# Performance work log

Measured on AMD Instinct MI355X. Metric: run time of the kernel, lower is better.

Reference implementation:

```python
import jax, jax.numpy as jnp
import numpy as np

B, N, C, H = 4, 1024, 768, 12
D = C // H
SCALE = D ** -0.5


def setup_inputs() -> dict:
    key = jax.random.key(0)
    k1, k2, k3, k4 = jax.random.split(key, 4)
    x1 = jax.random.normal(k1, (B, N, C), dtype=jnp.float32)
    x2 = jax.random.normal(k2, (B, N, C), dtype=jnp.float32)
    # shared (dual-stream) Linear2 weights, torch nn.Linear layout: [out, in]
    W_qkv = jax.random.normal(k3, (3 * C, C), dtype=jnp.float32) * (C ** -0.5)
    b_qkv = jnp.zeros((3 * C,), dtype=jnp.float32)
    W_proj = jax.random.normal(k4, (C, C), dtype=jnp.float32) * (C ** -0.5)
    b_proj = jnp.zeros((C,), dtype=jnp.float32)
    return {"x1": x1, "x2": x2, "W_qkv": W_qkv, "b_qkv": b_qkv,
            "W_proj": W_proj, "b_proj": b_proj}


def _split_qkv(x, W_qkv, b_qkv):
    qkv = (x @ W_qkv.T + b_qkv).reshape(B, N, 3, H, D)
    qkv = jnp.transpose(qkv, (2, 0, 3, 1, 4))  # [3,B,H,N,D]
    return qkv[0], qkv[1], qkv[2]


def reference(x1, x2, W_qkv, b_qkv, W_proj, b_proj):
    q1, k1, v1 = _split_qkv(x1, W_qkv, b_qkv)
    q2, k2, v2 = _split_qkv(x2, W_qkv, b_qkv)
    # two score maps, combined before a single shared softmax
    s1 = jnp.einsum("bhqd,bhkd->bhqk", q1 * SCALE, k1)
    s2 = jnp.einsum("bhqd,bhkd->bhqk", q2 * SCALE, k2)
    attn = jax.nn.softmax(s1 + s2, axis=-1)  # [B,H,N,N]
    # same attention matrix applied to both value streams
    o1 = jnp.einsum("bhqk,bhkd->bhqd", attn, v1)
    o2 = jnpum = jnp.einsum("bhqk,bhkd->bhqd", attn, v2) if False else jnp.einsum("bhqk,bhkd->bhqd", attn, v2)
    o1 = jnp.transpose(o1, (0, 2, 1, 3)).reshape(B, N, C)
    o2 = jnp.transpose(o2, (0, 2, 1, 3)).reshape(B, N, C)
    y1 = o1 @ W_proj.T + b_proj
    y2 = o2 @ W_proj.T + b_proj
    return y1, y2
```

## Files before the change

kernel.cpp:

```cpp
#include <hip/hip_runtime.h>
#include <hip/hip_bf16.h>


typedef __bf16 bf16x8 __attribute__((ext_vector_type(8)));
typedef __bf16 bf16x4 __attribute__((ext_vector_type(4)));
typedef float  f32x4  __attribute__((ext_vector_type(4)));

__device__ __forceinline__ bf16x8 cvt8(const float* p) {
    f32x4 f0 = *(const f32x4*)p;
    f32x4 f1 = *(const f32x4*)(p + 4);
    bf16x8 r;
    r[0] = (__bf16)f0[0]; r[1] = (__bf16)f0[1]; r[2] = (__bf16)f0[2]; r[3] = (__bf16)f0[3];
    r[4] = (__bf16)f1[0]; r[5] = (__bf16)f1[1]; r[6] = (__bf16)f1[2]; r[7] = (__bf16)f1[3];
    return r;
}

__device__ __forceinline__ void async16(const __bf16* g, __bf16* l) {
    __builtin_amdgcn_global_load_lds(
        (const __attribute__((address_space(1))) void*)g,
        (__attribute__((address_space(3))) void*)l, 16, 0, 0);
}

__global__ __launch_bounds__(256)
void cvt3_k(const float* __restrict__ x1, const float* __restrict__ x2,
            const float* __restrict__ wq, __bf16* __restrict__ xc,
            __bf16* __restrict__ wqc)
{
    int bid = blockIdx.x;
    const float* src; __bf16* dst; int i;
    if (bid < 1536)      { src = x1; dst = xc;             i = (bid * 256 + threadIdx.x) * 8; }
    else if (bid < 3072) { src = x2; dst = xc + 3145728;   i = ((bid - 1536) * 256 + threadIdx.x) * 8; }
    else                 { src = wq; dst = wqc;            i = ((bid - 3072) * 256 + threadIdx.x) * 8; }
    *(bf16x8*)(dst + i) = cvt8(src + i);
}

__global__ __launch_bounds__(256)
void cvt_k(const float* __restrict__ src, __bf16* __restrict__ dst, int n) {
    int i = (blockIdx.x * 256 + threadIdx.x) * 8;
    if (i < n) *(bf16x8*)(dst + i) = cvt8(src + i);
}

__global__ __launch_bounds__(256)
void gemm_qkv_s(const __bf16* __restrict__ Xc, const __bf16* __restrict__ Wq,
                const float* __restrict__ bias,
                __bf16* __restrict__ qo, __bf16* __restrict__ ko,
                __bf16* __restrict__ vo)
{
    constexpr int K = 768;
    __shared__ __bf16 As[3][128 * 32];
    __shared__ __bf16 Bs[3][128 * 32];

    const int t = threadIdx.x, w = t >> 6, lane = t & 63;
    const int l15 = lane & 15, quad = lane >> 4;
    const int wm = w >> 1, wn = w & 1;

    const int bid  = blockIdx.x;
    const int xcd  = bid & 7;
    const int i6   = bid >> 3;
    const int pair = i6 / 18;
    const int gx   = i6 - pair * 18;
    const int p    = xcd * 8 + pair;
    const int gy   = p & 31;
    const int st   = p >> 5;

    const int lrow = lane >> 2, lcol = (lane & 3) * 8;

    const __bf16* Ab = Xc + (size_t)st * 3145728 + (size_t)(gy * 128) * K;
    const __bf16* Bb = Wq + (size_t)(gx * 128) * K;

    f32x4 acc[4][4];
#pragma unroll
    for (int mi = 0; mi < 4; mi++)
#pragma unroll
        for (int ni = 0; ni < 4; ni++) acc[mi][ni] = f32x4{0.f, 0.f, 0.f, 0.f};

#pragma unroll
    for (int i = 0; i < 2; i++) {
        int r = w * 32 + i * 16 + lrow;
        async16(Ab + (size_t)r * K + lcol, &As[0][r * 32 + lcol]);
        async16(Bb + (size_t)r * K + lcol, &Bs[0][r * 32 + lcol]);
    }

#pragma unroll 3
    for (int kt = 0; kt < 24; kt++) {
        const int cb = kt % 3;
        if (kt < 23) {
            const int nb = (kt + 1) % 3;
            const int k0 = (kt + 1) * 32;
#pragma unroll
            for (int i = 0; i < 2; i++) {
                int r = w * 32 + i * 16 + lrow;
                async16(Ab + (size_t)r * K + k0 + lcol, &As[nb][r * 32 + lcol]);
                async16(Bb + (size_t)r * K + k0 + lcol, &Bs[nb][r * 32 + lcol]);
            }
            asm volatile("s_waitcnt vmcnt(4)" ::: "memory");
        } else {
            asm volatile("s_waitcnt vmcnt(0)" ::: "memory");
        }
        __builtin_amdgcn_s_barrier();
        __builtin_amdgcn_sched_barrier(0);

        bf16x8 af[4], bfr[4];
#pragma unroll
        for (int mi = 0; mi < 4; mi++)
            af[mi] = *(const bf16x8*)&As[cb][(wm * 64 + mi * 16 + l15) * 32 + quad * 8];
#pragma unroll
        for (int ni = 0; ni < 4; ni++)
            bfr[ni] = *(const bf16x8*)&Bs[cb][(wn * 64 + ni * 16 + l15) * 32 + quad * 8];
#pragma unroll
        for (int mi = 0; mi < 4; mi++)
#pragma unroll
            for (int ni = 0; ni < 4; ni++)
                acc[mi][ni] = __builtin_amdgcn_mfma_f32_16x16x32_bf16(af[mi], bfr[ni], acc[mi][ni], 0, 0, 0);
    }

    const int which = (gx * 128) / 768;

    if (which == 2) {
#pragma unroll
        for (int ni = 0; ni < 4; ni++) {
            int j = gx * 128 + wn * 64 + ni * 16 + l15;
            int c = j - 1536;
            int h = c >> 6, d = c & 63;
            float bj = bias[j];
#pragma unroll
            for (int mi = 0; mi < 4; mi++) {
                int row0 = gy * 128 + wm * 64 + mi * 16 + quad * 4;
                int b = row0 >> 10, tok0 = row0 & 1023;
                bf16x4 pv;
#pragma unroll
                for (int r = 0; r < 4; r++) pv[r] = (__bf16)(acc[mi][ni][r] + bj);
                *(bf16x4*)&vo[((size_t)((st * 4 + b) * 12 + h) * 64 + d) * 1024 + tok0] = pv;
            }
        }
    } else {
#pragma unroll
        for (int ni = 0; ni < 4; ni++) {
            int j     = gx * 128 + wn * 64 + ni * 16 + l15;
            int c     = j - which * 768;
            int h = c >> 6, d = c & 63;
            float bj  = bias[j];
#pragma unroll
            for (int mi = 0; mi < 4; mi++) {
#pragma unroll
                for (int r = 0; r < 4; r++) {
                    int row = gy * 128 + wm * 64 + mi * 16 + quad * 4 + r;
                    int b = row >> 10, tok = row & 1023;
                    float val = acc[mi][ni][r] + bj;
                    if (which == 0)
                        qo[((size_t)((st * 4 + b) * 12 + h) * 1024 + tok) * 64 + d] = (__bf16)(val * 0.125f);
                    else
                        ko[((size_t)((st * 4 + b) * 12 + h) * 1024 + tok) * 64 + d] = (__bf16)val;
                }
            }
        }
    }
}

__global__ __launch_bounds__(256)
void gemm_proj(const __bf16* __restrict__ A, const __bf16* __restrict__ Wp,
               const float* __restrict__ bias, float* __restrict__ out)
{
    constexpr int K = 768;
    __shared__ __bf16 As[3][128 * 32];
    __shared__ __bf16 Bs[3][128 * 32];

    const int t = threadIdx.x, w = t >> 6, lane = t & 63;
    const int l15 = lane & 15, quad = lane >> 4;
    const int wm = w >> 1, wn = w & 1;
    const int gx = blockIdx.x, gy = blockIdx.y;
    const int lrow = lane >> 2, lcol = (lane & 3) * 8;

    const __bf16* Ab = A  + (size_t)(gy * 128) * K;
    const __bf16* Bb = Wp + (size_t)(gx * 128) * K;

    f32x4 acc[4][4];
#pragma unroll
    for (int mi = 0; mi < 4; mi++)
#pragma unroll
        for (int ni = 0; ni < 4; ni++) acc[mi][ni] = f32x4{0.f, 0.f, 0.f, 0.f};

#pragma unroll
    for (int i = 0; i < 2; i++) {
        int r = w * 32 + i * 16 + lrow;
        async16(Ab + (size_t)r * K + lcol, &As[0][r * 32 + lcol]);
        async16(Bb + (size_t)r * K + lcol, &Bs[0][r * 32 + lcol]);
    }

#pragma unroll 3
    for (int kt = 0; kt < 24; kt++) {
        const int cb = kt % 3;
        if (kt < 23) {
            const int nb = (kt + 1) % 3;
            const int k0 = (kt + 1) * 32;
#pragma unroll
            for (int i = 0; i < 2; i++) {
                int r = w * 32 + i * 16 + lrow;
                async16(Ab + (size_t)r * K + k0 + lcol, &As[nb][r * 32 + lcol]);
                async16(Bb + (size_t)r * K + k0 + lcol, &Bs[nb][r * 32 + lcol]);
            }
            asm volatile("s_waitcnt vmcnt(4)" ::: "memory");
        } else {
            asm volatile("s_waitcnt vmcnt(0)" ::: "memory");
        }
        __builtin_amdgcn_s_barrier();
        __builtin_amdgcn_sched_barrier(0);

        bf16x8 af[4], bfr[4];
#pragma unroll
        for (int mi = 0; mi < 4; mi++)
            af[mi] = *(const bf16x8*)&As[cb][(wm * 64 + mi * 16 + l15) * 32 + quad * 8];
#pragma unroll
        for (int ni = 0; ni < 4; ni++)
            bfr[ni] = *(const bf16x8*)&Bs[cb][(wn * 64 + ni * 16 + l15) * 32 + quad * 8];
#pragma unroll
        for (int mi = 0; mi < 4; mi++)
#pragma unroll
            for (int ni = 0; ni < 4; ni++)
                acc[mi][ni] = __builtin_amdgcn_mfma_f32_16x16x32_bf16(af[mi], bfr[ni], acc[mi][ni], 0, 0, 0);
    }

#pragma unroll
    for (int ni = 0; ni < 4; ni++) {
        int col  = gx * 128 + wn * 64 + ni * 16 + l15;
        float bj = bias[col];
#pragma unroll
        for (int mi = 0; mi < 4; mi++)
#pragma unroll
            for (int r = 0; r < 4; r++) {
                int row = gy * 128 + wm * 64 + mi * 16 + quad * 4 + r;
                out[(size_t)row * 768 + col] = acc[mi][ni][r] + bj;
            }
    }
}

__global__ __launch_bounds__(128, 2)
void attn_k(const __bf16* __restrict__ qws, const __bf16* __restrict__ kws,
            const __bf16* __restrict__ vws, __bf16* __restrict__ ows)
{
    __shared__ __bf16 Ks[2][2][2][2][512];
    __shared__ __bf16 Vs[2][2][4][512];
    __shared__ __bf16 Ps[2][2][16 * 72];

    const int g  = blockIdx.x;
    const int qt = g / 48;
    const int bh = g % 48;
    const int b = bh / 12, h = bh % 12;
    const int t = threadIdx.x, w = t >> 6, lane = t & 63;
    const int l15 = lane & 15, quad = lane >> 4;

    const size_t head_off = (size_t)bh * 65536;
    const size_t ss       = (size_t)48 * 65536;

    bf16x8 qf[2][2][2];
#pragma unroll
    for (int set = 0; set < 2; set++)
#pragma unroll
        for (int s = 0; s < 2; s++)
#pragma unroll
            for (int kk = 0; kk < 2; kk++)
                qf[set][s][kk] = *(const bf16x8*)(qws + s * ss + head_off
                    + (size_t)(qt * 64 + w * 32 + set * 16 + l15) * 64 + kk * 32 + quad * 8);

    float lsum[2] = {0.f, 0.f};
    f32x4 accO[2][2][4];
#pragma unroll
    for (int set = 0; set < 2; set++)
#pragma unroll
        for (int s = 0; s < 2; s++)
#pragma unroll
            for (int mi = 0; mi < 4; mi++) accO[set][s][mi] = f32x4{0.f, 0.f, 0.f, 0.f};

    const __bf16* kbase = kws + head_off;
    const __bf16* vbase = vws + head_off;

#define STAGE_TILE(BUF, KEYB)                                                   \
    do {                                                                        \
        if (w == 0) {                                                           \
            _Pragma("unroll")                                                   \
            for (int i = 0; i < 8; i++) {                                       \
                const int s = i >> 2, kk = (i >> 1) & 1, mi = i & 1;            \
                async16(kbase + s * ss + (size_t)((KEYB) + mi * 16 + l15) * 64  \
                            + kk * 32 + quad * 8,                               \
                        &Ks[BUF][s][kk][mi][lane * 8]);                         \
            }                                                                   \
        } else {                                                                \
            _Pragma("unroll")                                                   \
            for (int i = 0; i < 8; i++) {                                       \
                const int s = i >> 2, mi = i & 3;                               \
                async16(vbase + s * ss + (size_t)(mi * 16 + l15) * 1024         \
                            + (KEYB) + quad * 8,                                \
                        &Vs[BUF][s][mi][lane * 8]);                             \
            }                                                                   \
        }                                                                       \
    } while (0)

    STAGE_TILE(0, 0);
    __syncthreads();

#pragma unroll 2
    for (int kt = 0; kt < 32; kt++) {
        const int cb = kt & 1, nb = cb ^ 1;

        if (kt < 31) STAGE_TILE(nb, (kt + 1) * 32);

        f32x4 accS[2][2];
#pragma unroll
        for (int set = 0; set < 2; set++)
#pragma unroll
            for (int mi = 0; mi < 2; mi++) accS[set][mi] = f32x4{0.f, 0.f, 0.f, 0.f};
        __builtin_amdgcn_s_setprio(1);
#pragma unroll
        for (int s = 0; s < 2; s++)
#pragma unroll
            for (int kk = 0; kk < 2; kk++) {
                bf16x8 kf0 = *(const bf16x8*)&Ks[cb][s][kk][0][lane * 8];
                bf16x8 kf1 = *(const bf16x8*)&Ks[cb][s][kk][1][lane * 8];
#pragma unroll
                for (int set = 0; set < 2; set++) {
                    accS[set][0] = __builtin_amdgcn_mfma_f32_16x16x32_bf16(kf0, qf[set][s][kk], accS[set][0], 0, 0, 0);
                    accS[set][1] = __builtin_amdgcn_mfma_f32_16x16x32_bf16(kf1, qf[set][s][kk], accS[set][1], 0, 0, 0);
                }
            }
        __builtin_amdgcn_s_setprio(0);

#pragma unroll
        for (int set = 0; set < 2; set++) {
            float rs = 0.f;
#pragma unroll
            for (int mi = 0; mi < 2; mi++) {
                bf16x4 pk;
#pragma unroll
                for (int r = 0; r < 4; r++) {
                    float pv = __expf(accS[set][mi][r]);
                    pk[r] = (__bf16)pv;
                    rs += pv;
                }
                *(bf16x4*)&Ps[w][set][l15 * 72 + mi * 16 + quad * 4] = pk;
            }
            lsum[set] += rs;
        }

        bf16x8 pa0 = *(const bf16x8*)&Ps[w][0][l15 * 72 + quad * 8];
        bf16x8 pa1 = *(const bf16x8*)&Ps[w][1][l15 * 72 + quad * 8];
        __builtin_amdgcn_s_setprio(1);
#pragma unroll
        for (int s = 0; s < 2; s++)
#pragma unroll
            for (int mi = 0; mi < 4; mi++) {
                bf16x8 vf = *(const bf16x8*)&Vs[cb][s][mi][lane * 8];
                accO[0][s][mi] = __builtin_amdgcn_mfma_f32_16x16x32_bf16(vf, pa0, accO[0][s][mi], 0, 0, 0);
                accO[1][s][mi] = __builtin_amdgcn_mfma_f32_16x16x32_bf16(vf, pa1, accO[1][s][mi], 0, 0, 0);
            }
        __builtin_amdgcn_s_setprio(0);

        __syncthreads();
    }
#undef STAGE_TILE

#pragma unroll
    for (int set = 0; set < 2; set++) {
        float l = lsum[set];
        l += __shfl_xor(l, 16);
        l += __shfl_xor(l, 32);
        float il = 1.f / l;

        const int tok = qt * 64 + w * 32 + set * 16 + l15;
#pragma unroll
        for (int s = 0; s < 2; s++)
#pragma unroll
            for (int mi = 0; mi < 4; mi++) {
                bf16x4 ov;
#pragma unroll
                for (int r = 0; r < 4; r++) ov[r] = (__bf16)(accO[set][s][mi][r] * il);
                *(bf16x4*)&ows[((size_t)((s * 4 + b) * 1024 + tok)) * 768
                               + h * 64 + mi * 16 + quad * 4] = ov;
            }
    }
}

extern "C" void kernel_launch(void* const* d_in, const int* in_sizes, int n_in,
                              void* d_out, int out_size, void* d_ws, size_t ws_size,
                              hipStream_t stream)
{
    const float* x1    = (const float*)d_in[0];
    const float* x2    = (const float*)d_in[1];
    const float* Wqkv  = (const float*)d_in[2];
    const float* bqkv  = (const float*)d_in[3];
    const float* Wproj = (const float*)d_in[4];
    const float* bproj = (const float*)d_in[5];
    float* out = (float*)d_out;

    const size_t qkv_elems = (size_t)2 * 4 * 12 * 1024 * 64;
    __bf16* q_ws = (__bf16*)d_ws;
    __bf16* k_ws = q_ws + qkv_elems;
    __bf16* v_ws = k_ws + qkv_elems;
    __bf16* pool = v_ws + qkv_elems;
    __bf16* Wqc  = pool + 3145728;
    __bf16* o_ws = pool;
    __bf16* Wpc  = q_ws;
    __bf16* Xc   = (__bf16*)d_out;

    cvt3_k<<<3936, 256, 0, stream>>>(x1, x2, Wqkv, Xc, Wqc);
    gemm_qkv_s<<<1152, 256, 0, stream>>>(Xc, Wqc, bqkv, q_ws, k_ws, v_ws);
    attn_k<<<768, 128, 0, stream>>>(q_ws, k_ws, v_ws, o_ws);
    cvt_k<<<288, 256, 0, stream>>>(Wproj, Wpc, 589824);
    gemm_proj<<<dim3(6, 64), 256, 0, stream>>>(o_ws, Wpc, bproj, out);
}
```

Baseline: 214.0 us.

## Deepen GEMM pipelines to four stages and fold proj-weight conversion into first kernel

Both GEMM kernels move from a 3-buffer, prefetch-distance-1 pipeline to a 4-buffer pipeline that prefetches two k-tiles ahead, with the waitcnt thresholds adjusted to match. This should hide more global-load latency at the cost of more LDS per block, which may reduce occupancy. Separately, when the workspace is large enough, the W_proj fp32-to-bf16 conversion moves into the initial conversion kernel, removing one kernel launch before the projection GEMM.

Result: no change. 211.9 us (-1.0%).

```diff
diff --git a/kernel.cpp b/kernel.cpp
--- a/kernel.cpp
+++ b/kernel.cpp
@@ -22,15 +22,17 @@
 }
 
 __global__ __launch_bounds__(256)
-void cvt3_k(const float* __restrict__ x1, const float* __restrict__ x2,
-            const float* __restrict__ wq, __bf16* __restrict__ xc,
-            __bf16* __restrict__ wqc)
+void cvt4_k(const float* __restrict__ x1, const float* __restrict__ x2,
+            const float* __restrict__ wq, const float* __restrict__ wp,
+            __bf16* __restrict__ xc, __bf16* __restrict__ wqc,
+            __bf16* __restrict__ wpc)
 {
     int bid = blockIdx.x;
     const float* src; __bf16* dst; int i;
     if (bid < 1536)      { src = x1; dst = xc;             i = (bid * 256 + threadIdx.x) * 8; }
     else if (bid < 3072) { src = x2; dst = xc + 3145728;   i = ((bid - 1536) * 256 + threadIdx.x) * 8; }
-    else                 { src = wq; dst = wqc;            i = ((bid - 3072) * 256 + threadIdx.x) * 8; }
+    else if (bid < 3936) { src = wq; dst = wqc;            i = ((bid - 3072) * 256 + threadIdx.x) * 8; }
+    else                 { src = wp; dst = wpc;            i = ((bid - 3936) * 256 + threadIdx.x) * 8; }
     *(bf16x8*)(dst + i) = cvt8(src + i);
 }
 
@@ -47,8 +49,8 @@
                 __bf16* __restrict__ vo)
 {
     constexpr int K = 768;
-    __shared__ __bf16 As[3][128 * 32];
-    __shared__ __bf16 Bs[3][128 * 32];
+    __shared__ __bf16 As[4][128 * 32];
+    __shared__ __bf16 Bs[4][128 * 32];
 
     const int t = threadIdx.x, w = t >> 6, lane = t & 63;
     const int l15 = lane & 15, quad = lane >> 4;
@@ -74,25 +76,27 @@
 #pragma unroll
         for (int ni = 0; ni < 4; ni++) acc[mi][ni] = f32x4{0.f, 0.f, 0.f, 0.f};
 
-#pragma unroll
-    for (int i = 0; i < 2; i++) {
-        int r = w * 32 + i * 16 + lrow;
-        async16(Ab + (size_t)r * K + lcol, &As[0][r * 32 + lcol]);
-        async16(Bb + (size_t)r * K + lcol, &Bs[0][r * 32 + lcol]);
-    }
-
-#pragma unroll 3
+#define QSTAGE(BUF, KT)                                                         \
+    do {                                                                        \
+        const int _k0 = (KT) * 32;                                              \
+        _Pragma("unroll")                                                       \
+        for (int i = 0; i < 2; i++) {                                           \
+            int r = w * 32 + i * 16 + lrow;                                     \
+            async16(Ab + (size_t)r * K + _k0 + lcol, &As[BUF][r * 32 + lcol]);  \
+            async16(Bb + (size_t)r * K + _k0 + lcol, &Bs[BUF][r * 32 + lcol]);  \
+        }                                                                       \
+    } while (0)
+
+    QSTAGE(0, 0);
+    QSTAGE(1, 1);
+
+#pragma unroll 4
     for (int kt = 0; kt < 24; kt++) {
-        const int cb = kt % 3;
-        if (kt < 23) {
-            const int nb = (kt + 1) % 3;
-            const int k0 = (kt + 1) * 32;
-#pragma unroll
-            for (int i = 0; i < 2; i++) {
-                int r = w * 32 + i * 16 + lrow;
-                async16(Ab + (size_t)r * K + k0 + lcol, &As[nb][r * 32 + lcol]);
-                async16(Bb + (size_t)r * K + k0 + lcol, &Bs[nb][r * 32 + lcol]);
-            }
+        const int cb = kt & 3;
+        if (kt < 22) {
+            QSTAGE((kt + 2) & 3, kt + 2);
+            asm volatile("s_waitcnt vmcnt(8)" ::: "memory");
+        } else if (kt == 22) {
             asm volatile("s_waitcnt vmcnt(4)" ::: "memory");
         } else {
             asm volatile("s_waitcnt vmcnt(0)" ::: "memory");
@@ -113,6 +117,7 @@
             for (int ni = 0; ni < 4; ni++)
                 acc[mi][ni] = __builtin_amdgcn_mfma_f32_16x16x32_bf16(af[mi], bfr[ni], acc[mi][ni], 0, 0, 0);
     }
+#undef QSTAGE
 
     const int which = (gx * 128) / 768;
 
@@ -162,8 +167,8 @@
                const float* __restrict__ bias, float* __restrict__ out)
 {
     constexpr int K = 768;
-    __shared__ __bf16 As[3][128 * 32];
-    __shared__ __bf16 Bs[3][128 * 32];
+    __shared__ __bf16 As[4][128 * 32];
+    __shared__ __bf16 Bs[4][128 * 32];
 
     const int t = threadIdx.x, w = t >> 6, lane = t & 63;
     const int l15 = lane & 15, quad = lane >> 4;
@@ -180,25 +185,27 @@
 #pragma unroll
         for (int ni = 0; ni < 4; ni++) acc[mi][ni] = f32x4{0.f, 0.f, 0.f, 0.f};
 
-#pragma unroll
-    for (int i = 0; i < 2; i++) {
-        int r = w * 32 + i * 16 + lrow;
-        async16(Ab + (size_t)r * K + lcol, &As[0][r * 32 + lcol]);
-        async16(Bb + (size_t)r * K + lcol, &Bs[0][r * 32 + lcol]);
-    }
-
-#pragma unroll 3
+#define PSTAGE(BUF, KT)                                                         \
+    do {                                                                        \
+        const int _k0 = (KT) * 32;                                              \
+        _Pragma("unroll")                                                       \
+        for (int i = 0; i < 2; i++) {                                           \
+            int r = w * 32 + i * 16 + lrow;                                     \
+            async16(Ab + (size_t)r * K + _k0 + lcol, &As[BUF][r * 32 + lcol]);  \
+            async16(Bb + (size_t)r * K + _k0 + lcol, &Bs[BUF][r * 32 + lcol]);  \
+        }                                                                       \
+    } while (0)
+
+    PSTAGE(0, 0);
+    PSTAGE(1, 1);
+
+#pragma unroll 4
     for (int kt = 0; kt < 24; kt++) {
-        const int cb = kt % 3;
-        if (kt < 23) {
-            const int nb = (kt + 1) % 3;
-            const int k0 = (kt + 1) * 32;
-#pragma unroll
-            for (int i = 0; i < 2; i++) {
-                int r = w * 32 + i * 16 + lrow;
-                async16(Ab + (size_t)r * K + k0 + lcol, &As[nb][r * 32 + lcol]);
-                async16(Bb + (size_t)r * K + k0 + lcol, &Bs[nb][r * 32 + lcol]);
-            }
+        const int cb = kt & 3;
+        if (kt < 22) {
+            PSTAGE((kt + 2) & 3, kt + 2);
+            asm volatile("s_waitcnt vmcnt(8)" ::: "memory");
+        } else if (kt == 22) {
             asm volatile("s_waitcnt vmcnt(4)" ::: "memory");
         } else {
             asm volatile("s_waitcnt vmcnt(0)" ::: "memory");
@@ -219,6 +226,7 @@
             for (int ni = 0; ni < 4; ni++)
                 acc[mi][ni] = __builtin_amdgcn_mfma_f32_16x16x32_bf16(af[mi], bfr[ni], acc[mi][ni], 0, 0, 0);
     }
+#undef PSTAGE
 
 #pragma unroll
     for (int ni = 0; ni < 4; ni++) {
@@ -398,12 +406,15 @@
     __bf16* pool = v_ws + qkv_elems;
     __bf16* Wqc  = pool + 3145728;
     __bf16* o_ws = pool;
-    __bf16* Wpc  = q_ws;
     __bf16* Xc   = (__bf16*)d_out;
 
-    cvt3_k<<<3936, 256, 0, stream>>>(x1, x2, Wqkv, Xc, Wqc);
+    const bool big = ws_size >= (size_t)(4 * qkv_elems + 589824) * sizeof(__bf16);
+    __bf16* Wpc = big ? (pool + qkv_elems)
+                      : q_ws;
+
+    cvt4_k<<<big ? 4224 : 3936, 256, 0, stream>>>(x1, x2, Wqkv, Wproj, Xc, Wqc, Wpc);
     gemm_qkv_s<<<1152, 256, 0, stream>>>(Xc, Wqc, bqkv, q_ws, k_ws, v_ws);
     attn_k<<<768, 128, 0, stream>>>(q_ws, k_ws, v_ws, o_ws);
-    cvt_k<<<288, 256, 0, stream>>>(Wproj, Wpc, 589824);
+    if (!big) cvt_k<<<288, 256, 0, stream>>>(Wproj, Wpc, 589824);
     gemm_proj<<<dim3(6, 64), 256, 0, stream>>>(o_ws, Wpc, bproj, out);
 }
```

## Use 256x256 tiles with 8-wave pipelined QKV GEMM and fold proj weight cast

Applied to the files above, without the earlier changes.

The QKV projection GEMM moves from 128x128 tiles with 4 waves to 256x256 tiles with 8 waves. It uses a 4-deep LDS buffer with staggered A/B staging, split half-steps and s_setprio around the MFMA blocks, aiming for more operand reuse and better overlap of loads with compute. When the workspace is large enough, the W_proj bf16 conversion is folded into the first conversion kernel, which removes one launch. The grid shrinks to 288 blocks, which may leave CUs underfilled, and the larger LDS footprint limits occupancy.

New measurement: 222.9 us. +4.2%, slower.

```diff
diff --git a/kernel.cpp b/kernel.cpp
--- a/kernel.cpp
+++ b/kernel.cpp
@@ -22,15 +22,17 @@
 }
 
 __global__ __launch_bounds__(256)
-void cvt3_k(const float* __restrict__ x1, const float* __restrict__ x2,
-            const float* __restrict__ wq, __bf16* __restrict__ xc,
-            __bf16* __restrict__ wqc)
+void cvt4_k(const float* __restrict__ x1, const float* __restrict__ x2,
+            const float* __restrict__ wq, const float* __restrict__ wp,
+            __bf16* __restrict__ xc, __bf16* __restrict__ wqc,
+            __bf16* __restrict__ wpc)
 {
     int bid = blockIdx.x;
     const float* src; __bf16* dst; int i;
     if (bid < 1536)      { src = x1; dst = xc;             i = (bid * 256 + threadIdx.x) * 8; }
     else if (bid < 3072) { src = x2; dst = xc + 3145728;   i = ((bid - 1536) * 256 + threadIdx.x) * 8; }
-    else                 { src = wq; dst = wqc;            i = ((bid - 3072) * 256 + threadIdx.x) * 8; }
+    else if (bid < 3936) { src = wq; dst = wqc;            i = ((bid - 3072) * 256 + threadIdx.x) * 8; }
+    else                 { src = wp; dst = wpc;            i = ((bid - 3936) * 256 + threadIdx.x) * 8; }
     *(bf16x8*)(dst + i) = cvt8(src + i);
 }
 
@@ -40,92 +42,125 @@
     if (i < n) *(bf16x8*)(dst + i) = cvt8(src + i);
 }
 
-__global__ __launch_bounds__(256)
-void gemm_qkv_s(const __bf16* __restrict__ Xc, const __bf16* __restrict__ Wq,
-                const float* __restrict__ bias,
-                __bf16* __restrict__ qo, __bf16* __restrict__ ko,
-                __bf16* __restrict__ vo)
+__global__ __launch_bounds__(512, 2)
+void gemm_qkv_8p(const __bf16* __restrict__ Xc, const __bf16* __restrict__ Wq,
+                 const float* __restrict__ bias,
+                 __bf16* __restrict__ qo, __bf16* __restrict__ ko,
+                 __bf16* __restrict__ vo)
 {
     constexpr int K = 768;
-    __shared__ __bf16 As[3][128 * 32];
-    __shared__ __bf16 Bs[3][128 * 32];
+    __shared__ __bf16 As[4][256 * 32];
+    __shared__ __bf16 Bs[4][256 * 32];
 
     const int t = threadIdx.x, w = t >> 6, lane = t & 63;
     const int l15 = lane & 15, quad = lane >> 4;
-    const int wm = w >> 1, wn = w & 1;
-
-    const int bid  = blockIdx.x;
-    const int xcd  = bid & 7;
-    const int i6   = bid >> 3;
-    const int pair = i6 / 18;
-    const int gx   = i6 - pair * 18;
-    const int p    = xcd * 8 + pair;
-    const int gy   = p & 31;
-    const int st   = p >> 5;
-
-    const int lrow = lane >> 2, lcol = (lane & 3) * 8;
-
-    const __bf16* Ab = Xc + (size_t)st * 3145728 + (size_t)(gy * 128) * K;
-    const __bf16* Bb = Wq + (size_t)(gx * 128) * K;
-
-    f32x4 acc[4][4];
-#pragma unroll
-    for (int mi = 0; mi < 4; mi++)
+    const int wm = w >> 2, wn = w & 3;
+
+    const int bid = blockIdx.x;
+    const int xcd = bid & 7;
+    const int i6  = bid >> 3;
+    const int gy  = xcd * 4 + i6 / 9;
+    const int gx  = i6 % 9;
+    const int st  = gy >> 4;
+    const int gyl = gy & 15;
+
+    const int srow = t >> 2, scol = (t & 3) * 8;
+
+    const __bf16* Ab = Xc + (size_t)st * 3145728 + (size_t)(gyl * 256) * K;
+    const __bf16* Bb = Wq + (size_t)(gx * 256) * K;
+
+    f32x4 acc[8][4];
+#pragma unroll
+    for (int mi = 0; mi < 8; mi++)
 #pragma unroll
         for (int ni = 0; ni < 4; ni++) acc[mi][ni] = f32x4{0.f, 0.f, 0.f, 0.f};
 
-#pragma unroll
-    for (int i = 0; i < 2; i++) {
-        int r = w * 32 + i * 16 + lrow;
-        async16(Ab + (size_t)r * K + lcol, &As[0][r * 32 + lcol]);
-        async16(Bb + (size_t)r * K + lcol, &Bs[0][r * 32 + lcol]);
-    }
-
-#pragma unroll 3
-    for (int kt = 0; kt < 24; kt++) {
-        const int cb = kt % 3;
-        if (kt < 23) {
-            const int nb = (kt + 1) % 3;
-            const int k0 = (kt + 1) * 32;
-#pragma unroll
-            for (int i = 0; i < 2; i++) {
-                int r = w * 32 + i * 16 + lrow;
-                async16(Ab + (size_t)r * K + k0 + lcol, &As[nb][r * 32 + lcol]);
-                async16(Bb + (size_t)r * K + k0 + lcol, &Bs[nb][r * 32 + lcol]);
-            }
-            asm volatile("s_waitcnt vmcnt(4)" ::: "memory");
-        } else {
-            asm volatile("s_waitcnt vmcnt(0)" ::: "memory");
-        }
-        __builtin_amdgcn_s_barrier();
-        __builtin_amdgcn_sched_barrier(0);
-
-        bf16x8 af[4], bfr[4];
-#pragma unroll
-        for (int mi = 0; mi < 4; mi++)
-            af[mi] = *(const bf16x8*)&As[cb][(wm * 64 + mi * 16 + l15) * 32 + quad * 8];
-#pragma unroll
-        for (int ni = 0; ni < 4; ni++)
-            bfr[ni] = *(const bf16x8*)&Bs[cb][(wn * 64 + ni * 16 + l15) * 32 + quad * 8];
-#pragma unroll
-        for (int mi = 0; mi < 4; mi++)
+#define STG_A(BF, K0)                                                            \
+    do {                                                                         \
+        async16(Ab + (size_t)srow * K + (K0) + scol,                             \
+                &As[BF][srow * 32 + scol]);                                      \
+        async16(Ab + (size_t)(128 + srow) * K + (K0) + scol,                     \
+                &As[BF][(128 + srow) * 32 + scol]);                              \
+    } while (0)
+#define STG_B(BF, K0)                                                            \
+    do {                                                                         \
+        async16(Bb + (size_t)srow * K + (K0) + scol,                             \
+                &Bs[BF][srow * 32 + scol]);                                      \
+        async16(Bb + (size_t)(128 + srow) * K + (K0) + scol,                     \
+                &Bs[BF][(128 + srow) * 32 + scol]);                              \
+    } while (0)
+
+    STG_A(0, 0); STG_B(0, 0);
+    STG_A(1, 32); STG_B(1, 32);
+    asm volatile("s_waitcnt vmcnt(4)" ::: "memory");
+    __builtin_amdgcn_s_barrier();
+    __builtin_amdgcn_sched_barrier(0);
+
+#pragma unroll 4
+    for (int g = 0; g < 24; g++) {
+        const int bf = g & 3;
+        const int sb = (g + 2) & 3;
+        const int sk = (g + 2) * 32;
+        bf16x8 bfr[4];
+
+        {
+            bf16x8 af[4];
+#pragma unroll
+            for (int mi = 0; mi < 4; mi++)
+                af[mi] = *(const bf16x8*)&As[bf][(wm * 128 + mi * 16 + l15) * 32 + quad * 8];
 #pragma unroll
             for (int ni = 0; ni < 4; ni++)
-                acc[mi][ni] = __builtin_amdgcn_mfma_f32_16x16x32_bf16(af[mi], bfr[ni], acc[mi][ni], 0, 0, 0);
-    }
-
-    const int which = (gx * 128) / 768;
+                bfr[ni] = *(const bf16x8*)&Bs[bf][(wn * 64 + ni * 16 + l15) * 32 + quad * 8];
+            if (g < 22) STG_A(sb, sk);
+            __builtin_amdgcn_s_barrier();
+            __builtin_amdgcn_sched_barrier(0);
+            __builtin_amdgcn_s_setprio(1);
+#pragma unroll
+            for (int mi = 0; mi < 4; mi++)
+#pragma unroll
+                for (int ni = 0; ni < 4; ni++)
+                    acc[mi][ni] = __builtin_amdgcn_mfma_f32_16x16x32_bf16(af[mi], bfr[ni], acc[mi][ni], 0, 0, 0);
+            __builtin_amdgcn_s_setprio(0);
+            __builtin_amdgcn_s_barrier();
+            __builtin_amdgcn_sched_barrier(0);
+        }
+
+        {
+            bf16x8 af[4];
+#pragma unroll
+            for (int mi = 0; mi < 4; mi++)
+                af[mi] = *(const bf16x8*)&As[bf][(wm * 128 + 64 + mi * 16 + l15) * 32 + quad * 8];
+            if (g < 22) STG_B(sb, sk);
+            __builtin_amdgcn_s_barrier();
+            __builtin_amdgcn_sched_barrier(0);
+            __builtin_amdgcn_s_setprio(1);
+#pragma unroll
+            for (int mi = 0; mi < 4; mi++)
+#pragma unroll
+                for (int ni = 0; ni < 4; ni++)
+                    acc[4 + mi][ni] = __builtin_amdgcn_mfma_f32_16x16x32_bf16(af[mi], bfr[ni], acc[4 + mi][ni], 0, 0, 0);
+            __builtin_amdgcn_s_setprio(0);
+            if (g < 22)       { asm volatile("s_waitcnt vmcnt(4)" ::: "memory"); }
+            else if (g == 22) { asm volatile("s_waitcnt vmcnt(0)" ::: "memory"); }
+            __builtin_amdgcn_s_barrier();
+            __builtin_amdgcn_sched_barrier(0);
+        }
+    }
+#undef STG_A
+#undef STG_B
+
+    const int which = gx / 3;
 
     if (which == 2) {
 #pragma unroll
         for (int ni = 0; ni < 4; ni++) {
-            int j = gx * 128 + wn * 64 + ni * 16 + l15;
+            int j = gx * 256 + wn * 64 + ni * 16 + l15;
             int c = j - 1536;
             int h = c >> 6, d = c & 63;
             float bj = bias[j];
 #pragma unroll
-            for (int mi = 0; mi < 4; mi++) {
-                int row0 = gy * 128 + wm * 64 + mi * 16 + quad * 4;
+            for (int mi = 0; mi < 8; mi++) {
+                int row0 = gyl * 256 + wm * 128 + mi * 16 + quad * 4;
                 int b = row0 >> 10, tok0 = row0 & 1023;
                 bf16x4 pv;
 #pragma unroll
@@ -136,15 +171,15 @@
     } else {
 #pragma unroll
         for (int ni = 0; ni < 4; ni++) {
-            int j     = gx * 128 + wn * 64 + ni * 16 + l15;
-            int c     = j - which * 768;
+            int j = gx * 256 + wn * 64 + ni * 16 + l15;
+            int c = j - which * 768;
             int h = c >> 6, d = c & 63;
-            float bj  = bias[j];
-#pragma unroll
-            for (int mi = 0; mi < 4; mi++) {
+            float bj = bias[j];
+#pragma unroll
+            for (int mi = 0; mi < 8; mi++) {
 #pragma unroll
                 for (int r = 0; r < 4; r++) {
-                    int row = gy * 128 + wm * 64 + mi * 16 + quad * 4 + r;
+                    int row = gyl * 256 + wm * 128 + mi * 16 + quad * 4 + r;
                     int b = row >> 10, tok = row & 1023;
                     float val = acc[mi][ni][r] + bj;
                     if (which == 0)
@@ -398,12 +433,15 @@
     __bf16* pool = v_ws + qkv_elems;
     __bf16* Wqc  = pool + 3145728;
     __bf16* o_ws = pool;
-    __bf16* Wpc  = q_ws;
     __bf16* Xc   = (__bf16*)d_out;
 
-    cvt3_k<<<3936, 256, 0, stream>>>(x1, x2, Wqkv, Xc, Wqc);
-    gemm_qkv_s<<<1152, 256, 0, stream>>>(Xc, Wqc, bqkv, q_ws, k_ws, v_ws);
+    const bool big = ws_size >= (size_t)(4 * qkv_elems + 589824) * sizeof(__bf16);
+    __bf16* Wpc = big ? (pool + qkv_elems)
+                      : q_ws;
+
+    cvt4_k<<<big ? 4224 : 3936, 256, 0, stream>>>(x1, x2, Wqkv, Wproj, Xc, Wqc, Wpc);
+    gemm_qkv_8p<<<288, 512, 0, stream>>>(Xc, Wqc, bqkv, q_ws, k_ws, v_ws);
     attn_k<<<768, 128, 0, stream>>>(q_ws, k_ws, v_ws, o_ws);
-    cvt_k<<<288, 256, 0, stream>>>(Wproj, Wpc, 589824);
+    if (!big) cvt_k<<<288, 256, 0, stream>>>(Wproj, Wpc, 589824);
     gemm_proj<<<dim3(6, 64), 256, 0, stream>>>(o_ws, Wpc, bproj, out);
 }
```
